# Optimization experiments

Hardware: AMD Instinct MI355X
Metric: run time of the kernel (lower is better)

## Reference

```python
import jax, jax.numpy as jnp
import numpy as np

N, F_IN, F_OUT = 8192, 512, 64
LEAKY_ALPHA = 0.2
NEG_MASK = -9e15


def setup_inputs() -> dict:
    key = jax.random.key(0)
    k1, k2, k3, k4 = jax.random.split(key, 4)
    x = jax.random.normal(k1, (N, F_IN), dtype=jnp.float32)
    adj = jax.random.randint(k2, (N, N), 0, 2, dtype=jnp.int32)
    # xavier-normal-ish scale for params
    W = jax.random.normal(k3, (F_IN, F_OUT), dtype=jnp.float32) * np.sqrt(2.0 / (F_IN + F_OUT)).astype(np.float32)
    a = jax.random.normal(k4, (2 * F_OUT, 1), dtype=jnp.float32) * np.sqrt(2.0 / (2 * F_OUT + 1)).astype(np.float32)
    return {"x": x, "adj": adj, "W": W, "a": a}


def reference(x, adj, W, a):
    # eval mode: dropout is identity
    Wh = x @ W                                   # [N, F_out]
    wh_i = Wh @ a[:F_OUT, :]                     # [N, 1]
    wh_j = Wh @ a[F_OUT:, :]                     # [N, 1]
    e = wh_i + wh_j.T                            # [N, N] broadcast add
    e = jnp.where(e >= 0, e, LEAKY_ALPHA * e)    # leaky_relu
    e = jnp.where(adj > 0, e, NEG_MASK)
    attn = jax.nn.softmax(e, axis=1)             # row-wise softmax
    h = attn @ Wh                                # [N, F_out]
    # ELU activation
    return jax.nn.elu(h)
```

## Files before the change

### kernel.cpp

```cpp
#include <hip/hip_runtime.h>

#define NN 8192
#define FIN 512
#define FO 64

typedef short bf16x8 __attribute__((ext_vector_type(8)));
typedef float f32x4 __attribute__((ext_vector_type(4)));

union AFrag { bf16x8 v; __bf16 b[8]; };

__global__ void wt_kernel(const float* __restrict__ W, __bf16* __restrict__ WT) {
    const int f = blockIdx.x;
    const int k = threadIdx.x;
    WT[f * FIN + k] = (__bf16)W[k * FO + f];
}

__global__ __launch_bounds__(128) void wh_kernel(
    const float* __restrict__ x, const __bf16* __restrict__ WT,
    const float* __restrict__ a, uint4* __restrict__ whs,
    float* __restrict__ s_out, float* __restrict__ t_out)
{
    __shared__ float whlds[2][16][FO + 1];
    const int w  = threadIdx.x >> 6;
    const int l  = threadIdx.x & 63;
    const int lr = l & 15, lg = l >> 4;
    const int rb = (blockIdx.x * 2 + w) * 16;

    f32x4 acc[4] = {};
    const float* xr = x + (size_t)(rb + lr) * FIN;
    const __bf16* wbase[4];
    #pragma unroll
    for (int ft = 0; ft < 4; ++ft) wbase[ft] = WT + (ft*16 + lr) * FIN;

    for (int ks = 0; ks < 16; ++ks) {
        const int k0 = ks*32 + lg*4;
        const float4 xa = *(const float4*)(xr + k0);
        const float4 xb = *(const float4*)(xr + k0 + 16);
        AFrag af;
        af.b[0]=(__bf16)xa.x; af.b[1]=(__bf16)xa.y; af.b[2]=(__bf16)xa.z; af.b[3]=(__bf16)xa.w;
        af.b[4]=(__bf16)xb.x; af.b[5]=(__bf16)xb.y; af.b[6]=(__bf16)xb.z; af.b[7]=(__bf16)xb.w;
        #pragma unroll
        for (int ft = 0; ft < 4; ++ft) {
            union { bf16x8 v; uint2 q[2]; } bf;
            bf.q[0] = *(const uint2*)(wbase[ft] + k0);
            bf.q[1] = *(const uint2*)(wbase[ft] + k0 + 16);
            acc[ft] = __builtin_amdgcn_mfma_f32_16x16x32_bf16(af.v, bf.v, acc[ft], 0, 0, 0);
        }
    }

    #pragma unroll
    for (int ft = 0; ft < 4; ++ft)
        #pragma unroll
        for (int q = 0; q < 4; ++q)
            whlds[w][lg*4+q][ft*16+lr] = acc[ft][q];

    float sp[4] = {0,0,0,0}, tp[4] = {0,0,0,0};
    #pragma unroll
    for (int ft = 0; ft < 4; ++ft) {
        const float a1 = a[ft*16 + lr];
        const float a2 = a[FO + ft*16 + lr];
        #pragma unroll
        for (int q = 0; q < 4; ++q) { sp[q] += acc[ft][q]*a1; tp[q] += acc[ft][q]*a2; }
    }
    #pragma unroll
    for (int d = 1; d < 16; d <<= 1) {
        #pragma unroll
        for (int q = 0; q < 4; ++q) { sp[q] += __shfl_xor(sp[q], d); tp[q] += __shfl_xor(tp[q], d); }
    }
    if (lr == 0) {
        *(float4*)(s_out + rb + lg*4) = make_float4(sp[0], sp[1], sp[2], sp[3]);
        *(float4*)(t_out + rb + lg*4) = make_float4(tp[0], tp[1], tp[2], tp[3]);
    }

    __syncthreads();

    const int jb = blockIdx.x;
    #pragma unroll
    for (int q = 0; q < 2; ++q) {
        const int ft = w*2 + q;
        const int f  = ft*16 + lr;
        unsigned u[4];
        #pragma unroll
        for (int h = 0; h < 4; ++h) {
            const int c0 = ((h & 2) ? 16 : 0) + lg*4 + (h & 1)*2;
            union { __bf16 b; unsigned short us; } lo, hi;
            lo.b = (__bf16)whlds[c0 >> 4][c0 & 15][f];
            hi.b = (__bf16)whlds[(c0+1) >> 4][(c0+1) & 15][f];
            u[h] = (unsigned)lo.us | ((unsigned)hi.us << 16);
        }
        whs[(jb*4 + ft)*64 + l] = make_uint4(u[0], u[1], u[2], u[3]);
    }
}

__global__ __launch_bounds__(1024, 8) void gat_kernel(
    const int* __restrict__ adj, const uint4* __restrict__ whs,
    const float* __restrict__ s_in, const float* __restrict__ t_in,
    float* __restrict__ out)
{
    __shared__ float red[16][16][FO];
    __shared__ float dnl[16][16];
    const int w  = threadIdx.x >> 6;
    const int l  = threadIdx.x & 63;
    const int lr = l & 15, lg = l >> 4;
    const int rg = blockIdx.x;
    const int R  = rg * 16 + lr;
    const float sv = s_in[R];
    const int* adjr = adj + (size_t)R * NN;
    const bf16x8* wv = (const bf16x8*)whs;

    f32x4 acc[4] = {};
    float dn = 0.f;

    #pragma unroll 2
    for (int st = 0; st < 16; ++st) {
        const int jc = w*512 + st*32 + lg*4;
        const int jb = w*16 + st;

        const int4   A0 = *(const int4*)(adjr + jc);
        const int4   A1 = *(const int4*)(adjr + jc + 16);
        const float4 T0 = *(const float4*)(t_in + jc);
        const float4 T1 = *(const float4*)(t_in + jc + 16);

        const int   av[8] = {A0.x, A0.y, A0.z, A0.w, A1.x, A1.y, A1.z, A1.w};
        const float tv[8] = {T0.x, T0.y, T0.z, T0.w, T1.x, T1.y, T1.z, T1.w};
        float p[8];
        #pragma unroll
        for (int i = 0; i < 8; ++i) {
            float e = sv + tv[i];
            e = fmaxf(e, 0.2f * e);
            p[i] = av[i] ? __expf(e) : 0.f;
            dn += p[i];
        }
        AFrag af;
        #pragma unroll
        for (int i = 0; i < 8; ++i) af.b[i] = (__bf16)p[i];
        #pragma unroll
        for (int ft = 0; ft < 4; ++ft) {
            const bf16x8 bv = wv[(jb*4 + ft)*64 + l];
            acc[ft] = __builtin_amdgcn_mfma_f32_16x16x32_bf16(af.v, bv, acc[ft], 0, 0, 0);
        }
    }

    dn += __shfl_xor(dn, 16);
    dn += __shfl_xor(dn, 32);

    #pragma unroll
    for (int ft = 0; ft < 4; ++ft)
        #pragma unroll
        for (int q = 0; q < 4; ++q)
            red[w][lg*4+q][ft*16+lr] = acc[ft][q];
    if (l < 16) dnl[w][l] = dn;
    __syncthreads();

    {
        const int row = threadIdx.x >> 6, f = threadIdx.x & 63;
        float v = 0.f, den = 0.f;
        #pragma unroll
        for (int ww = 0; ww < 16; ++ww) { v += red[ww][row][f]; den += dnl[ww][row]; }
        const float h = v / den;
        out[(size_t)(rg*16 + row) * FO + f] = (h > 0.f) ? h : (__expf(h) - 1.f);
    }
}

extern "C" void kernel_launch(void* const* d_in, const int* in_sizes, int n_in,
                              void* d_out, int out_size, void* d_ws, size_t ws_size,
                              hipStream_t stream) {
    const float* x   = (const float*)d_in[0];
    const int*   adj = (const int*)d_in[1];
    const float* W   = (const float*)d_in[2];
    const float* a   = (const float*)d_in[3];
    float* out = (float*)d_out;

    char* ws = (char*)d_ws;
    uint4*  whs = (uint4*)ws;
    __bf16* WT  = (__bf16*)(ws + (1u << 20));
    float*  s   = (float*)(ws + (1u << 20) + (1u << 16));
    float*  t   = (float*)(ws + (1u << 20) + (1u << 16) + 32768);

    wt_kernel<<<64, 512, 0, stream>>>(W, WT);
    wh_kernel<<<256, 128, 0, stream>>>(x, WT, a, whs, s, t);
    gat_kernel<<<512, 1024, 0, stream>>>(adj, whs, s, t, out);
}
```

Before: 95.46 us.

## Software-pipeline adj/t/Wh loads in GAT kernel and restructure block work split

The GAT kernel now uses 512-thread blocks that each handle 32 rows, with 4 waves splitting the columns per row group. Inside the loop, adj is prefetched 4 steps ahead, t 2 steps ahead and the Wh fragments 1 step ahead through register ring buffers, to hide HBM latency on the dominant adj stream. The WT transpose now goes through an LDS tile so both reads and writes are coalesced, and the wh_kernel prefetches x one step ahead. The added prefetch registers raise register pressure and the grid halves to 256 blocks, which may reduce occupancy.

```diff
diff --git a/kernel.cpp b/kernel.cpp
--- a/kernel.cpp
+++ b/kernel.cpp
@@ -9,10 +9,27 @@
 
 union AFrag { bf16x8 v; __bf16 b[8]; };
 
-__global__ void wt_kernel(const float* __restrict__ W, __bf16* __restrict__ WT) {
-    const int f = blockIdx.x;
-    const int k = threadIdx.x;
-    WT[f * FIN + k] = (__bf16)W[k * FO + f];
+__global__ __launch_bounds__(512) void wt_kernel(const float* __restrict__ W, __bf16* __restrict__ WT) {
+    __shared__ float tile[64][65];
+    const int k0 = blockIdx.x * 64;
+    #pragma unroll
+    for (int r = 0; r < 8; ++r) {
+        const int kl = r * 8 + (threadIdx.x >> 6);
+        const int f  = threadIdx.x & 63;
+        tile[kl][f] = W[(size_t)(k0 + kl) * FO + f];
+    }
+    __syncthreads();
+    const int f   = threadIdx.x >> 3;
+    const int kk8 = (threadIdx.x & 7) * 8;
+    unsigned u[4];
+    #pragma unroll
+    for (int h = 0; h < 4; ++h) {
+        union { __bf16 b; unsigned short us; } lo, hi;
+        lo.b = (__bf16)tile[kk8 + 2*h][f];
+        hi.b = (__bf16)tile[kk8 + 2*h + 1][f];
+        u[h] = (unsigned)lo.us | ((unsigned)hi.us << 16);
+    }
+    *(uint4*)(WT + (size_t)f * FIN + k0 + kk8) = make_uint4(u[0], u[1], u[2], u[3]);
 }
 
 __global__ __launch_bounds__(128) void wh_kernel(
@@ -32,10 +49,14 @@
     #pragma unroll
     for (int ft = 0; ft < 4; ++ft) wbase[ft] = WT + (ft*16 + lr) * FIN;
 
+    float4 nxa = *(const float4*)(xr + lg*4);
+    float4 nxb = *(const float4*)(xr + lg*4 + 16);
     for (int ks = 0; ks < 16; ++ks) {
         const int k0 = ks*32 + lg*4;
-        const float4 xa = *(const float4*)(xr + k0);
-        const float4 xb = *(const float4*)(xr + k0 + 16);
+        const float4 xa = nxa, xb = nxb;
+        const int kn = (ks < 15 ? ks + 1 : 15)*32 + lg*4;
+        nxa = *(const float4*)(xr + kn);
+        nxb = *(const float4*)(xr + kn + 16);
         AFrag af;
         af.b[0]=(__bf16)xa.x; af.b[1]=(__bf16)xa.y; af.b[2]=(__bf16)xa.z; af.b[3]=(__bf16)xa.w;
         af.b[4]=(__bf16)xb.x; af.b[5]=(__bf16)xb.y; af.b[6]=(__bf16)xb.z; af.b[7]=(__bf16)xb.w;
@@ -92,34 +113,65 @@
     }
 }
 
-__global__ __launch_bounds__(1024, 8) void gat_kernel(
+__global__ __launch_bounds__(512, 4) void gat_kernel(
     const int* __restrict__ adj, const uint4* __restrict__ whs,
     const float* __restrict__ s_in, const float* __restrict__ t_in,
     float* __restrict__ out)
 {
-    __shared__ float red[16][16][FO];
-    __shared__ float dnl[16][16];
+    __shared__ float red[8][16][FO];
+    __shared__ float dnl[8][16];
     const int w  = threadIdx.x >> 6;
+    const int g  = w >> 2;
+    const int kw = w & 3;
     const int l  = threadIdx.x & 63;
     const int lr = l & 15, lg = l >> 4;
     const int rg = blockIdx.x;
-    const int R  = rg * 16 + lr;
+    const int R  = rg * 32 + g * 16 + lr;
     const float sv = s_in[R];
     const int* adjr = adj + (size_t)R * NN;
     const bf16x8* wv = (const bf16x8*)whs;
+    const int cbase = kw * 2048 + lg * 4;
+    const int jbase = kw * 64;
 
     f32x4 acc[4] = {};
     float dn = 0.f;
 
-    #pragma unroll 2
-    for (int st = 0; st < 16; ++st) {
-        const int jc = w*512 + st*32 + lg*4;
-        const int jb = w*16 + st;
-
-        const int4   A0 = *(const int4*)(adjr + jc);
-        const int4   A1 = *(const int4*)(adjr + jc + 16);
-        const float4 T0 = *(const float4*)(t_in + jc);
-        const float4 T1 = *(const float4*)(t_in + jc + 16);
+    int4   pa[4][2];
+    float4 pt[2][2];
+    bf16x8 bv[2][4];
+
+    #pragma unroll
+    for (int i = 0; i < 4; ++i) {
+        const int jc = cbase + i*32;
+        pa[i][0] = *(const int4*)(adjr + jc);
+        pa[i][1] = *(const int4*)(adjr + jc + 16);
+    }
+    #pragma unroll
+    for (int i = 0; i < 2; ++i) {
+        const int jc = cbase + i*32;
+        pt[i][0] = *(const float4*)(t_in + jc);
+        pt[i][1] = *(const float4*)(t_in + jc + 16);
+    }
+    #pragma unroll
+    for (int ft = 0; ft < 4; ++ft) bv[0][ft] = wv[(jbase*4 + ft)*64 + l];
+
+    #pragma unroll 4
+    for (int st = 0; st < 64; ++st) {
+        const int sl4 = st & 3, sl2 = st & 1;
+        const int4   A0 = pa[sl4][0], A1 = pa[sl4][1];
+        const float4 T0 = pt[sl2][0], T1 = pt[sl2][1];
+
+        {
+            const int ja = cbase + (st+4 < 64 ? st+4 : 63)*32;
+            pa[sl4][0] = *(const int4*)(adjr + ja);
+            pa[sl4][1] = *(const int4*)(adjr + ja + 16);
+            const int jt = cbase + (st+2 < 64 ? st+2 : 63)*32;
+            pt[sl2][0] = *(const float4*)(t_in + jt);
+            pt[sl2][1] = *(const float4*)(t_in + jt + 16);
+            const int jbn = jbase + (st+1 < 64 ? st+1 : 63);
+            #pragma unroll
+            for (int ft = 0; ft < 4; ++ft) bv[(st+1)&1][ft] = wv[(jbn*4 + ft)*64 + l];
+        }
 
         const int   av[8] = {A0.x, A0.y, A0.z, A0.w, A1.x, A1.y, A1.z, A1.w};
         const float tv[8] = {T0.x, T0.y, T0.z, T0.w, T1.x, T1.y, T1.z, T1.w};
@@ -135,10 +187,8 @@
         #pragma unroll
         for (int i = 0; i < 8; ++i) af.b[i] = (__bf16)p[i];
         #pragma unroll
-        for (int ft = 0; ft < 4; ++ft) {
-            const bf16x8 bv = wv[(jb*4 + ft)*64 + l];
-            acc[ft] = __builtin_amdgcn_mfma_f32_16x16x32_bf16(af.v, bv, acc[ft], 0, 0, 0);
-        }
+        for (int ft = 0; ft < 4; ++ft)
+            acc[ft] = __builtin_amdgcn_mfma_f32_16x16x32_bf16(af.v, bv[st&1][ft], acc[ft], 0, 0, 0);
     }
 
     dn += __shfl_xor(dn, 16);
@@ -152,13 +202,14 @@
     if (l < 16) dnl[w][l] = dn;
     __syncthreads();
 
-    {
-        const int row = threadIdx.x >> 6, f = threadIdx.x & 63;
+    for (int o = threadIdx.x; o < 32*FO; o += 512) {
+        const int row = o >> 6, f = o & 63;
+        const int gg = row >> 4, r16 = row & 15;
         float v = 0.f, den = 0.f;
         #pragma unroll
-        for (int ww = 0; ww < 16; ++ww) { v += red[ww][row][f]; den += dnl[ww][row]; }
+        for (int ww = 0; ww < 4; ++ww) { v += red[gg*4+ww][r16][f]; den += dnl[gg*4+ww][r16]; }
         const float h = v / den;
-        out[(size_t)(rg*16 + row) * FO + f] = (h > 0.f) ? h : (__expf(h) - 1.f);
+        out[(size_t)(rg*32 + row) * FO + f] = (h > 0.f) ? h : (__expf(h) - 1.f);
     }
 }
 
@@ -177,7 +228,7 @@
     float*  s   = (float*)(ws + (1u << 20) + (1u << 16));
     float*  t   = (float*)(ws + (1u << 20) + (1u << 16) + 32768);
 
-    wt_kernel<<<64, 512, 0, stream>>>(W, WT);
+    wt_kernel<<<8, 512, 0, stream>>>(W, WT);
     wh_kernel<<<256, 128, 0, stream>>>(x, WT, a, whs, s, t);
-    gat_kernel<<<512, 1024, 0, stream>>>(adj, whs, s, t, out);
-}
+    gat_kernel<<<256, 512, 0, stream>>>(adj, whs, s, t, out);
+}
```

Result: slower. 156.9 us (+64.4%).
